# Optimization experiments

Measured on AMD Instinct MI355X. Metric: run time of the kernel, lower is better.

Reference implementation:

```python
import jax, jax.numpy as jnp
import numpy as np

# AdaptiveLogSoftmaxWithLoss config (input_dim=2048, n_classes=50257, div_value=4.0)
CUTOFFS = [1000, 10000, 50257]  # torch appends n_classes
N_CLUSTERS = 2                   # len(CUTOFFS) - 1
HEAD_SIZE = CUTOFFS[0] + N_CLUSTERS  # 1002
D = 2048
HSZ = [D // 4, D // 16]          # tail hidden sizes: [512, 128]
N_TOK = 4096


def setup_inputs() -> dict:
    key = jax.random.key(0)
    ks = jax.random.split(key, 7)
    w = 0.02  # weight scale so logits stay O(1)
    x = jax.random.normal(ks[0], (N_TOK, D), dtype=jnp.float32)
    W_head = jax.random.normal(ks[1], (HEAD_SIZE, D), dtype=jnp.float32) * w
    W1_0 = jax.random.normal(ks[2], (HSZ[0], D), dtype=jnp.float32) * w
    W2_0 = jax.random.normal(ks[3], (CUTOFFS[1] - CUTOFFS[0], HSZ[0]), dtype=jnp.float32) * w  # [9000, 512]
    W1_1 = jax.random.normal(ks[4], (HSZ[1], D), dtype=jnp.float32) * w
    W2_1 = jax.random.normal(ks[5], (CUTOFFS[2] - CUTOFFS[1], HSZ[1]), dtype=jnp.float32) * w  # [40257, 128]
    target = jax.random.randint(ks[6], (N_TOK,), 0, CUTOFFS[2], dtype=jnp.int32)
    return {"x": x, "target": target, "W_head": W_head,
            "W1_0": W1_0, "W2_0": W2_0, "W1_1": W1_1, "W2_1": W2_1}


def reference(x, target, W_head, W1_0, W2_0, W1_1, W2_1):
    # head: [N, 1002] = [1000 frequent classes | 2 cluster logits]
    head = x @ W_head.T
    head_lsm = jax.nn.log_softmax(head, axis=-1)

    t = target
    # log-prob of target if it lies in the head (clip keeps gather in-range; masked later)
    head_lp = jnp.take_along_axis(head_lsm, jnp.clip(t, 0, CUTOFFS[0] - 1)[:, None], axis=1)[:, 0]

    def tail_target_lp(W1, W2, low, high, cluster_idx):
        # two-stage projection: [N,D] @ [D,h] @ [h,osz]
        logits = (x @ W1.T) @ W2.T                     # [N, high-low]
        lsm = jax.nn.log_softmax(logits, axis=-1)
        idx = jnp.clip(t - low, 0, high - low - 1)
        g = jnp.take_along_axis(lsm, idx[:, None], axis=1)[:, 0]
        # combine with head's cluster log-prob
        return head_lsm[:, CUTOFFS[0] + cluster_idx] + g

    lp0 = tail_target_lp(W1_0, W2_0, CUTOFFS[0], CUTOFFS[1], 0)
    lp1 = tail_target_lp(W1_1, W2_1, CUTOFFS[1], CUTOFFS[2], 1)

    out = jnp.where(t < CUTOFFS[0], head_lp, jnp.where(t < CUTOFFS[1], lp0, lp1))
    loss = -jnp.mean(out)
    return out, loss
```

## Files before the change

### kernel.cpp

```cpp
#include <hip/hip_runtime.h>
#include <hip/hip_bf16.h>
#include <math.h>

#define NTOK 4096
#define DIM 2048
#define NHEAD 1002
#define NCAT 1664
#define C0LO 1000
#define C0HI 10000
#define OSZ0 9000
#define OSZ1 40257
#define H0S 512
#define H1S 128
#define JS0 24
#define JS1 16
#define HEADBLKS 8
#define NT0 71
#define NT1 315
#define PROJB 416
#define CVTB 448

typedef __attribute__((ext_vector_type(4))) short short4v;
typedef __attribute__((ext_vector_type(8))) short short8v;
typedef __attribute__((ext_vector_type(4))) float f32x4;
typedef __hip_bfloat16 bf16;

#define GLOBAL_AS __attribute__((address_space(1)))
#define LDS_AS __attribute__((address_space(3)))

#define RAW_BAR() __builtin_amdgcn_s_barrier()
#define SCHED_FENCE() __builtin_amdgcn_sched_barrier(0)
#define WAIT_VM(N) asm volatile("s_waitcnt vmcnt(" #N ")" ::: "memory")
#define WAIT_LGKM0() asm volatile("s_waitcnt lgkmcnt(0)" ::: "memory")

__device__ __forceinline__ int kperm(int c) {
  return (c & ~31) | (((c & 15) >> 2) << 3) | (((c >> 4) & 1) << 2) | (c & 3);
}

__device__ __forceinline__ void cvt8(const float* s1, const float* s2, bf16* dst) {
  union { short8v v; bf16 h[8]; } u;
  float4 a = *reinterpret_cast<const float4*>(s1);
  float4 b = *reinterpret_cast<const float4*>(s2);
  u.h[0] = __float2bfloat16(a.x); u.h[1] = __float2bfloat16(a.y);
  u.h[2] = __float2bfloat16(a.z); u.h[3] = __float2bfloat16(a.w);
  u.h[4] = __float2bfloat16(b.x); u.h[5] = __float2bfloat16(b.y);
  u.h[6] = __float2bfloat16(b.z); u.h[7] = __float2bfloat16(b.w);
  *reinterpret_cast<short8v*>(dst) = u.v;
}

__global__ __launch_bounds__(256) void cvt_xw(
    const float* __restrict__ x, const float* __restrict__ W_head,
    const float* __restrict__ W1_0, const float* __restrict__ W1_1,
    bf16* __restrict__ xb, bf16* __restrict__ Wcat) {
  const long NX = (long)NTOK * DIM / 8;
  const long NC = (long)NCAT * DIM / 8;
  long gid = (long)blockIdx.x * 256 + threadIdx.x;
  if (gid < NX) {
    long rel = gid * 8;
    long c1 = (rel & ~31L) + ((rel >> 3) & 3) * 4;
    cvt8(x + c1, x + c1 + 16, xb + rel);
  } else if (gid < NX + NC) {
    long rel = (gid - NX) * 8;
    int row = (int)(rel >> 11);
    long c1 = (rel & ~31L) + ((rel >> 3) & 3) * 4;
    int col = (int)(c1 & 2047);
    const float* srow = nullptr;
    if (row < NHEAD) srow = W_head + (long)row * DIM;
    else if (row < 1024) srow = nullptr;
    else if (row < 1536) srow = W1_0 + (long)(row - 1024) * DIM;
    else srow = W1_1 + (long)(row - 1536) * DIM;
    if (srow) {
      cvt8(srow + col, srow + col + 16, Wcat + rel);
    } else {
      union { short8v v; bf16 h[8]; } u;
#pragma unroll
      for (int e = 0; e < 8; ++e) u.h[e] = __float2bfloat16(0.f);
      *reinterpret_cast<short8v*>(Wcat + rel) = u.v;
    }
  }
}

__device__ __forceinline__ void stage_tile(const bf16* __restrict__ g, int row0,
                                           int maxrow, int ld, int k0,
                                           char* lds, int wave, int lane) {
#pragma unroll
  for (int c = 0; c < 4; ++c) {
    int rbase = wave * 32 + c * 8;
    int row = rbase + (lane >> 3);
    int grow = row0 + row;
    grow = grow < maxrow ? grow : maxrow;
    int slot = (lane & 7) ^ (row & 7);
    const bf16* src = g + (size_t)grow * ld + k0 + slot * 8;
    __builtin_amdgcn_global_load_lds((const GLOBAL_AS unsigned int*)src,
                                     (LDS_AS unsigned int*)(lds + rbase * 128),
                                     16, 0, 0);
  }
}

__device__ __forceinline__ short8v read_frag(const char* lds, int row, int kk, int lane) {
  int slot = (kk * 4 + (lane >> 4)) ^ (row & 7);
  return *reinterpret_cast<const short8v*>(lds + row * 128 + slot * 16);
}

__device__ __forceinline__ void stage_tile256(const bf16* __restrict__ g, int row0,
                                              int maxrow, int ld,
                                              char* lds, int wave, int lane) {
#pragma unroll
  for (int c = 0; c < 8; ++c) {
    int rbase = wave * 32 + c * 4;
    int row = rbase + (lane >> 4);
    int grow = row0 + row;
    grow = grow < maxrow ? grow : maxrow;
    int slot = (lane & 15) ^ (row & 7);
    const bf16* src = g + (size_t)grow * ld + slot * 8;
    __builtin_amdgcn_global_load_lds((const GLOBAL_AS unsigned int*)src,
                                     (LDS_AS unsigned int*)(lds + rbase * 256),
                                     16, 0, 0);
  }
}

__device__ __forceinline__ short8v read_frag256(const char* lds, int row, int kk, int lane) {
  int slot = (kk * 4 + (lane >> 4)) ^ (row & 7);
  return *reinterpret_cast<const short8v*>(lds + row * 256 + slot * 16);
}

__device__ __forceinline__ void reduce_write_ps(float srun[4][4], float* reds,
                                                float* ps, int slice, int tok0,
                                                int lane, int wr, int wc) {
#pragma unroll
  for (int off = 1; off < 16; off <<= 1)
#pragma unroll
    for (int m = 0; m < 4; ++m)
#pragma unroll
      for (int r = 0; r < 4; ++r) srun[m][r] += __shfl_xor(srun[m][r], off);
  __syncthreads();
  if (wc == 0 && (lane & 15) == 0) {
#pragma unroll
    for (int m = 0; m < 4; ++m)
#pragma unroll
      for (int r = 0; r < 4; ++r)
        reds[wr * 64 + m * 16 + (lane >> 4) * 4 + r] = srun[m][r];
  }
  __syncthreads();
  if (wc == 1 && (lane & 15) == 0) {
#pragma unroll
    for (int m = 0; m < 4; ++m)
#pragma unroll
      for (int r = 0; r < 4; ++r) {
        int row = wr * 64 + m * 16 + (lane >> 4) * 4 + r;
        ps[(size_t)slice * NTOK + tok0 + row] = reds[row] + srun[m][r];
      }
  }
}

__global__ __launch_bounds__(256, 3) void tail0_lse(
    const bf16* __restrict__ Ab, const bf16* __restrict__ W2b,
    float* __restrict__ ps) {
  __shared__ __align__(16) char As[128 * 128];
  __shared__ __align__(16) char Bs[128 * 128];
  __shared__ float reds[128];
  int tid = threadIdx.x;
  int lane = tid & 63, wave = tid >> 6;
  int wr = wave >> 1, wc = wave & 1;
  int tok0 = blockIdx.x * 128;
  int ys = blockIdx.y;
  int t_lo = (NT0 * ys) / JS0, t_hi = (NT0 * (ys + 1)) / JS0;
  float srun[4][4] = {};
  for (int jt = t_lo; jt < t_hi; ++jt) {
    int j0 = jt * 128;
    f32x4 acc[4][4] = {};
    for (int k0 = 0; k0 < H0S; k0 += 64) {
      __syncthreads();
      stage_tile(Ab, tok0, NTOK - 1, H0S, k0, As, wave, lane);
      stage_tile(W2b, j0, OSZ0 - 1, H0S, k0, Bs, wave, lane);
      __syncthreads();
#pragma unroll
      for (int kk = 0; kk < 2; ++kk) {
        short8v af[4], bfr[4];
#pragma unroll
        for (int m = 0; m < 4; ++m)
          af[m] = read_frag(As, wr * 64 + m * 16 + (lane & 15), kk, lane);
#pragma unroll
        for (int n = 0; n < 4; ++n)
          bfr[n] = read_frag(Bs, wc * 64 + n * 16 + (lane & 15), kk, lane);
#pragma unroll
        for (int m = 0; m < 4; ++m)
#pragma unroll
          for (int n = 0; n < 4; ++n)
            acc[m][n] = __builtin_amdgcn_mfma_f32_16x16x32_bf16(af[m], bfr[n], acc[m][n], 0, 0, 0);
      }
    }
#pragma unroll
    for (int m = 0; m < 4; ++m)
#pragma unroll
      for (int n = 0; n < 4; ++n) {
        int col = j0 + wc * 64 + n * 16 + (lane & 15);
        if (col < OSZ0) {
#pragma unroll
          for (int r = 0; r < 4; ++r) srun[m][r] += __expf(acc[m][n][r]);
        }
      }
  }
  reduce_write_ps(srun, reds, ps, ys, tok0, lane, wr, wc);
}

__device__ void tail1_body(const bf16* __restrict__ Ab, const bf16* __restrict__ W2b,
                           float* __restrict__ ps, char* lds) {
  char* buf0 = lds;
  char* buf1 = lds + 32768;
  float* reds = (float*)(lds + 65536);
  int tid = threadIdx.x;
  int lane = tid & 63, wave = tid >> 6;
  int wr = wave >> 1, wc = wave & 1;
  int tok0 = blockIdx.x * 128;
  int ys = blockIdx.y;
  int t_lo = (NT1 * ys) / JS1, t_hi = (NT1 * (ys + 1)) / JS1;
  int nt = t_hi - t_lo;

  stage_tile256(Ab, tok0, NTOK - 1, H1S, buf1, wave, lane);
  WAIT_VM(0); SCHED_FENCE();
  RAW_BAR();
  short8v afr[4][4];
#pragma unroll
  for (int kk = 0; kk < 4; ++kk)
#pragma unroll
    for (int m = 0; m < 4; ++m)
      afr[kk][m] = read_frag256(buf1, wr * 64 + m * 16 + (lane & 15), kk, lane);
  stage_tile256(W2b, t_lo * 128, OSZ1 - 1, H1S, buf0, wave, lane);
  WAIT_LGKM0(); SCHED_FENCE();
  RAW_BAR();
  if (nt > 1) stage_tile256(W2b, (t_lo + 1) * 128, OSZ1 - 1, H1S, buf1, wave, lane);

  float srun[4][4] = {};
  for (int i = 0; i < nt; ++i) {
    char* cur = (i & 1) ? buf1 : buf0;
    if (i + 1 < nt) { WAIT_VM(8); } else { WAIT_VM(0); }
    SCHED_FENCE();
    RAW_BAR();
    int j0 = (t_lo + i) * 128;
    f32x4 acc[4][4] = {};
#pragma unroll
    for (int kk = 0; kk < 4; ++kk) {
      short8v bfr[4];
#pragma unroll
      for (int n = 0; n < 4; ++n)
        bfr[n] = read_frag256(cur, wc * 64 + n * 16 + (lane & 15), kk, lane);
#pragma unroll
      for (int m = 0; m < 4; ++m)
#pragma unroll
        for (int n = 0; n < 4; ++n)
          acc[m][n] = __builtin_amdgcn_mfma_f32_16x16x32_bf16(afr[kk][m], bfr[n], acc[m][n], 0, 0, 0);
    }
#pragma unroll
    for (int m = 0; m < 4; ++m)
#pragma unroll
      for (int n = 0; n < 4; ++n) {
        int col = j0 + wc * 64 + n * 16 + (lane & 15);
        if (col < OSZ1) {
#pragma unroll
          for (int r = 0; r < 4; ++r) srun[m][r] += __expf(acc[m][n][r]);
        }
      }
    SCHED_FENCE();
    RAW_BAR();
    if (i + 2 < nt) stage_tile256(W2b, (t_lo + i + 2) * 128, OSZ1 - 1, H1S, cur, wave, lane);
  }
  reduce_write_ps(srun, reds, ps, ys, tok0, lane, wr, wc);
}

__global__ __launch_bounds__(256, 2) void tail1_lse(
    const bf16* __restrict__ Ab, const bf16* __restrict__ W2b,
    float* __restrict__ ps) {
  __shared__ __align__(16) char lds[66048];
  tail1_body(Ab, W2b, ps, lds);
}

__global__ __launch_bounds__(256, 3) void proj_plus(
    const bf16* __restrict__ A, const bf16* __restrict__ B,
    const float* __restrict__ W2_0, const float* __restrict__ W2_1,
    bf16* __restrict__ W20b, bf16* __restrict__ W21b,
    float* __restrict__ head, float* __restrict__ h0, bf16* __restrict__ h0b,
    float* __restrict__ h1, bf16* __restrict__ h1b, float* __restrict__ ps_head) {
  __shared__ __align__(16) char As[16384];
  __shared__ __align__(16) char Bs[16384];
  __shared__ float reds[128];
  if (blockIdx.x >= PROJB) {
    const long N20 = (long)OSZ0 * H0S / 8;
    const long N21 = (long)OSZ1 * H1S / 8;
    long idx = (long)(blockIdx.x - PROJB) * 256 + threadIdx.x;
    const long stride = (long)CVTB * 256;
    for (; idx < N20 + N21; idx += stride) {
      long rel; const float* srcb; bf16* dstb;
      if (idx < N20) { rel = idx * 8;          srcb = W2_0; dstb = W20b; }
      else           { rel = (idx - N20) * 8;  srcb = W2_1; dstb = W21b; }
      long c1 = (rel & ~31L) + ((rel >> 3) & 3) * 4;
      cvt8(srcb + c1, srcb + c1 + 16, dstb + rel);
    }
    return;
  }
  int tid = threadIdx.x;
  int lane = tid & 63, wave = tid >> 6;
  int wr = wave >> 1, wc = wave & 1;
  int wgid = blockIdx.x;
  int cx = wgid & 7, w = wgid >> 3;
  int col_b = w >> 2;
  int row_b = cx * 4 + (w & 3);
  int row0 = row_b * 128, col0 = col_b * 128;
  f32x4 acc[4][4] = {};
  for (int k0 = 0; k0 < DIM; k0 += 64) {
    __syncthreads();
    stage_tile(A, row0, NTOK - 1, DIM, k0, As, wave, lane);
    stage_tile(B, col0, NCAT - 1, DIM, k0, Bs, wave, lane);
    __syncthreads();
#pragma unroll
    for (int kk = 0; kk < 2; ++kk) {
      short8v af[4], bfr[4];
#pragma unroll
      for (int m = 0; m < 4; ++m)
        af[m] = read_frag(As, wr * 64 + m * 16 + (lane & 15), kk, lane);
#pragma unroll
      for (int n = 0; n < 4; ++n)
        bfr[n] = read_frag(Bs, wc * 64 + n * 16 + (lane & 15), kk, lane);
#pragma unroll
      for (int m = 0; m < 4; ++m)
#pragma unroll
        for (int n = 0; n < 4; ++n)
          acc[m][n] = __builtin_amdgcn_mfma_f32_16x16x32_bf16(af[m], bfr[n], acc[m][n], 0, 0, 0);
    }
  }
  float srun[4][4] = {};
#pragma unroll
  for (int m = 0; m < 4; ++m) {
    int row = row0 + wr * 64 + m * 16 + (lane >> 4) * 4;
#pragma unroll
    for (int n = 0; n < 4; ++n) {
      int col = col0 + wc * 64 + n * 16 + (lane & 15);
#pragma unroll
      for (int r = 0; r < 4; ++r) {
        float v = acc[m][n][r];
        if (col < NHEAD) {
          head[(size_t)(row + r) * NHEAD + col] = v;
          srun[m][r] += __expf(v);
        } else if (col >= 1024 && col < 1536) {
          int c = col - 1024;
          h0[(size_t)(row + r) * H0S + c] = v;
          h0b[(size_t)(row + r) * H0S + kperm(c)] = __float2bfloat16(v);
        } else if (col >= 1536) {
          int c = col - 1536;
          h1[(size_t)(row + r) * H1S + c] = v;
          h1b[(size_t)(row + r) * H1S + kperm(c)] = __float2bfloat16(v);
        }
      }
    }
  }
  if (col_b < HEADBLKS) {
    reduce_write_ps(srun, reds, ps_head, col_b, row0, lane, wr, wc);
  }
}

__global__ __launch_bounds__(256) void finalize2(
    const int* __restrict__ target, const float* __restrict__ head,
    const float* __restrict__ ps_head,
    const float* __restrict__ h0, const float* __restrict__ h1,
    const float* __restrict__ W2_0, const float* __restrict__ W2_1,
    const float* __restrict__ ps0, const float* __restrict__ ps1,
    float* __restrict__ out) {
  int warp = threadIdx.x >> 6, lane = threadIdx.x & 63;
  int i = blockIdx.x * 4 + warp;
  if (i >= NTOK) return;
  int t = target[i];
  float sh = 0.f;
#pragma unroll
  for (int s = 0; s < HEADBLKS; ++s) sh += ps_head[(size_t)s * NTOK + i];
  float lse_head = logf(sh);
  float res;
  if (t < C0LO) {
    res = head[(size_t)i * NHEAD + t] - lse_head;
  } else {
    int c = (t < C0HI) ? 0 : 1;
    int H = c ? H1S : H0S;
    int low = c ? C0HI : C0LO;
    const float* hv = (c ? h1 : h0) + (size_t)i * H;
    const float* wv = (c ? W2_1 : W2_0) + (size_t)(t - low) * H;
    float p = 0.f;
    for (int k = lane * 4; k < H; k += 256) {
      float4 a = *reinterpret_cast<const float4*>(hv + k);
      float4 b = *reinterpret_cast<const float4*>(wv + k);
      p += a.x * b.x + a.y * b.y + a.z * b.z + a.w * b.w;
    }
#pragma unroll
    for (int off = 32; off > 0; off >>= 1) p += __shfl_xor(p, off);
    const float* ps = c ? ps1 : ps0;
    int js = c ? JS1 : JS0;
    float S = 0.f;
    for (int s = 0; s < js; ++s) S += ps[(size_t)s * NTOK + i];
    float cl = head[(size_t)i * NHEAD + C0LO + c];
    res = (cl - lse_head) + (p - logf(S));
  }
  if (lane == 0) out[i] = res;
}

__global__ __launch_bounds__(256) void loss_kernel(float* __restrict__ out) {
  __shared__ float red[256];
  int tid = threadIdx.x;
  float s = 0.f;
  for (int j = tid; j < NTOK; j += 256) s += out[j];
  red[tid] = s; __syncthreads();
  for (int off = 128; off > 0; off >>= 1) {
    if (tid < off) red[tid] += red[tid + off];
    __syncthreads();
  }
  if (tid == 0) out[NTOK] = -red[0] / (float)NTOK;
}

extern "C" void kernel_launch(void* const* d_in, const int* in_sizes, int n_in,
                              void* d_out, int out_size, void* d_ws, size_t ws_size,
                              hipStream_t stream) {
  (void)in_sizes; (void)n_in; (void)out_size; (void)ws_size;
  const float* x = (const float*)d_in[0];
  const int* target = (const int*)d_in[1];
  const float* W_head = (const float*)d_in[2];
  const float* W1_0 = (const float*)d_in[3];
  const float* W2_0 = (const float*)d_in[4];
  const float* W1_1 = (const float*)d_in[5];
  const float* W2_1 = (const float*)d_in[6];
  float* out = (float*)d_out;

  char* w = (char*)d_ws;
  size_t off = 0;
  auto alloc = [&](size_t bytes) -> void* {
    void* p = w + off;
    off = (off + bytes + 255) & ~(size_t)255;
    return p;
  };
  bf16* xb   = (bf16*)alloc((size_t)NTOK * DIM * 2);
  bf16* Wcat = (bf16*)alloc((size_t)NCAT * DIM * 2);
  bf16* W20b = (bf16*)alloc((size_t)OSZ0 * H0S * 2);
  bf16* W21b = (bf16*)alloc((size_t)OSZ1 * H1S * 2);
  float* head = (float*)alloc((size_t)NTOK * NHEAD * 4);
  float* h0   = (float*)alloc((size_t)NTOK * H0S * 4);
  bf16*  h0b  = (bf16*)alloc((size_t)NTOK * H0S * 2);
  float* h1   = (float*)alloc((size_t)NTOK * H1S * 4);
  bf16*  h1b  = (bf16*)alloc((size_t)NTOK * H1S * 2);
  float* ps_head = (float*)alloc((size_t)HEADBLKS * NTOK * 4);
  float* ps0 = (float*)alloc((size_t)JS0 * NTOK * 4);
  float* ps1 = (float*)alloc((size_t)JS1 * NTOK * 4);

  dim3 blk(256);
  const long NXW = (long)NTOK * DIM / 8 + (long)NCAT * DIM / 8;
  cvt_xw<<<dim3((unsigned)((NXW + 255) / 256)), blk, 0, stream>>>(
      x, W_head, W1_0, W1_1, xb, Wcat);

  proj_plus<<<dim3(PROJB + CVTB), blk, 0, stream>>>(
      xb, Wcat, W2_0, W2_1, W20b, W21b, head, h0, h0b, h1, h1b, ps_head);

  tail0_lse<<<dim3(NTOK / 128, JS0), blk, 0, stream>>>(h0b, W20b, ps0);
  tail1_lse<<<dim3(NTOK / 128, JS1), blk, 0, stream>>>(h1b, W21b, ps1);

  finalize2<<<dim3(NTOK / 4), blk, 0, stream>>>(target, head, ps_head, h0, h1,
                                                W2_0, W2_1, ps0, ps1, out);
  loss_kernel<<<1, blk, 0, stream>>>(out);
}
```

Measured before the change: 179.5 us.

## Double-buffer tail0 LSE GEMM tiles with async prefetch two stages ahead

Rewrites the tail0 log-sum-exp GEMM loop as a flattened, double-buffered pipeline. Each k-step waits on vmcnt and a raw barrier while the tile loads for two steps ahead are already issued, so global loads overlap the MFMA work. Previously every k-step paid two full syncthreads around the staging loads. LDS use doubles to about 64KB, so occupancy drops from 3 to 2 blocks per CU, and the j-slice count and a convert block constant are retuned to match.

```diff
diff --git a/kernel.cpp b/kernel.cpp
--- a/kernel.cpp
+++ b/kernel.cpp
@@ -12,13 +12,13 @@
 #define OSZ1 40257
 #define H0S 512
 #define H1S 128
-#define JS0 24
+#define JS0 16
 #define JS1 16
 #define HEADBLKS 8
 #define NT0 71
 #define NT1 315
 #define PROJB 416
-#define CVTB 448
+#define CVTB 352
 
 typedef __attribute__((ext_vector_type(4))) short short4v;
 typedef __attribute__((ext_vector_type(8))) short short8v;
@@ -153,55 +153,84 @@
   }
 }
 
-__global__ __launch_bounds__(256, 3) void tail0_lse(
-    const bf16* __restrict__ Ab, const bf16* __restrict__ W2b,
-    float* __restrict__ ps) {
-  __shared__ __align__(16) char As[128 * 128];
-  __shared__ __align__(16) char Bs[128 * 128];
-  __shared__ float reds[128];
+__device__ void tail0_body(const bf16* __restrict__ Ab, const bf16* __restrict__ W2b,
+                           float* __restrict__ ps, char* lds) {
+  char* Abuf[2] = {lds, lds + 16384};
+  char* Bbuf[2] = {lds + 32768, lds + 49152};
+  float* reds = (float*)(lds + 65536);
   int tid = threadIdx.x;
   int lane = tid & 63, wave = tid >> 6;
   int wr = wave >> 1, wc = wave & 1;
   int tok0 = blockIdx.x * 128;
   int ys = blockIdx.y;
   int t_lo = (NT0 * ys) / JS0, t_hi = (NT0 * (ys + 1)) / JS0;
+  int niter = (t_hi - t_lo) * 8;
+
+  stage_tile(Ab, tok0, NTOK - 1, H0S, 0, Abuf[0], wave, lane);
+  stage_tile(W2b, t_lo * 128, OSZ0 - 1, H0S, 0, Bbuf[0], wave, lane);
+  if (niter > 1) {
+    stage_tile(Ab, tok0, NTOK - 1, H0S, 64, Abuf[1], wave, lane);
+    stage_tile(W2b, t_lo * 128, OSZ0 - 1, H0S, 64, Bbuf[1], wave, lane);
+  }
   float srun[4][4] = {};
-  for (int jt = t_lo; jt < t_hi; ++jt) {
-    int j0 = jt * 128;
-    f32x4 acc[4][4] = {};
-    for (int k0 = 0; k0 < H0S; k0 += 64) {
-      __syncthreads();
-      stage_tile(Ab, tok0, NTOK - 1, H0S, k0, As, wave, lane);
-      stage_tile(W2b, j0, OSZ0 - 1, H0S, k0, Bs, wave, lane);
-      __syncthreads();
-#pragma unroll
-      for (int kk = 0; kk < 2; ++kk) {
-        short8v af[4], bfr[4];
-#pragma unroll
-        for (int m = 0; m < 4; ++m)
-          af[m] = read_frag(As, wr * 64 + m * 16 + (lane & 15), kk, lane);
+  f32x4 acc[4][4];
+  for (int it = 0; it < niter; ++it) {
+    char* Ac = Abuf[it & 1];
+    char* Bc = Bbuf[it & 1];
+    if (it + 1 < niter) { WAIT_VM(8); } else { WAIT_VM(0); }
+    SCHED_FENCE();
+    RAW_BAR();
+    int kst = it & 7;
+    if (kst == 0) {
+#pragma unroll
+      for (int m = 0; m < 4; ++m)
+#pragma unroll
+        for (int n = 0; n < 4; ++n) acc[m][n] = f32x4{0.f, 0.f, 0.f, 0.f};
+    }
+#pragma unroll
+    for (int kk = 0; kk < 2; ++kk) {
+      short8v af[4], bfr[4];
+#pragma unroll
+      for (int m = 0; m < 4; ++m)
+        af[m] = read_frag(Ac, wr * 64 + m * 16 + (lane & 15), kk, lane);
+#pragma unroll
+      for (int n = 0; n < 4; ++n)
+        bfr[n] = read_frag(Bc, wc * 64 + n * 16 + (lane & 15), kk, lane);
+#pragma unroll
+      for (int m = 0; m < 4; ++m)
 #pragma unroll
         for (int n = 0; n < 4; ++n)
-          bfr[n] = read_frag(Bs, wc * 64 + n * 16 + (lane & 15), kk, lane);
-#pragma unroll
-        for (int m = 0; m < 4; ++m)
-#pragma unroll
-          for (int n = 0; n < 4; ++n)
-            acc[m][n] = __builtin_amdgcn_mfma_f32_16x16x32_bf16(af[m], bfr[n], acc[m][n], 0, 0, 0);
-      }
-    }
-#pragma unroll
-    for (int m = 0; m < 4; ++m)
-#pragma unroll
-      for (int n = 0; n < 4; ++n) {
-        int col = j0 + wc * 64 + n * 16 + (lane & 15);
-        if (col < OSZ0) {
-#pragma unroll
-          for (int r = 0; r < 4; ++r) srun[m][r] += __expf(acc[m][n][r]);
+          acc[m][n] = __builtin_amdgcn_mfma_f32_16x16x32_bf16(af[m], bfr[n], acc[m][n], 0, 0, 0);
+    }
+    if (kst == 7) {
+      int j0 = (t_lo + (it >> 3)) * 128;
+#pragma unroll
+      for (int m = 0; m < 4; ++m)
+#pragma unroll
+        for (int n = 0; n < 4; ++n) {
+          int col = j0 + wc * 64 + n * 16 + (lane & 15);
+          if (col < OSZ0) {
+#pragma unroll
+            for (int r = 0; r < 4; ++r) srun[m][r] += __expf(acc[m][n][r]);
+          }
         }
-      }
+    }
+    SCHED_FENCE();
+    RAW_BAR();
+    if (it + 2 < niter) {
+      int it2 = it + 2;
+      stage_tile(Ab, tok0, NTOK - 1, H0S, (it2 & 7) * 64, Ac, wave, lane);
+      stage_tile(W2b, (t_lo + (it2 >> 3)) * 128, OSZ0 - 1, H0S, (it2 & 7) * 64, Bc, wave, lane);
+    }
   }
   reduce_write_ps(srun, reds, ps, ys, tok0, lane, wr, wc);
+}
+
+__global__ __launch_bounds__(256, 2) void tail0_lse(
+    const bf16* __restrict__ Ab, const bf16* __restrict__ W2b,
+    float* __restrict__ ps) {
+  __shared__ __align__(16) char lds[66048];
+  tail0_body(Ab, W2b, ps, lds);
 }
 
 __device__ void tail1_body(const bf16* __restrict__ Ab, const bf16* __restrict__ W2b,
```

New measurement: 176.4 us. About the same (-1.7%).
